# Performance work log

Hardware: AMD Instinct MI355X
Metric: run time of the kernel (lower is better)

The kernel has to match this reference:

```python
import jax, jax.numpy as jnp
import numpy as np

N, K, D, DOUT = 100000, 16, 128, 128

def setup_inputs() -> dict:
    key = jax.random.key(0)
    k1, k2, k3 = jax.random.split(key, 3)
    self_vecs = jax.random.normal(k1, (N, D), dtype=jnp.float32)
    neigh_vecs = jax.random.normal(k2, (N, K, D), dtype=jnp.float32)
    # glorot([input_dim, output_dim])
    limit = np.sqrt(6.0 / (D + DOUT)).astype(np.float32)
    weights = jax.random.uniform(k3, (D, DOUT), dtype=jnp.float32, minval=-limit, maxval=limit)
    return {"self_vecs": self_vecs, "neigh_vecs": neigh_vecs, "weights": weights}

def reference(self_vecs, neigh_vecs, weights):
    # concat self node as an extra "neighbor": [N, K+1, D]
    neigh_self = jnp.concatenate([neigh_vecs, self_vecs[:, None, :]], axis=1)
    # attention scores: query is the self vector, keys are neighbors+self -> [N, K+1]
    score = jnp.einsum('nd,nkd->nk', self_vecs, neigh_self)
    attn = jax.nn.softmax(score, axis=-1)
    # weighted sum of values -> [N, D]
    context = jnp.einsum('nk,nkd->nd', attn, neigh_self)
    out = context @ weights  # [N, DOUT]
    return jax.nn.relu(out)
```

## Files before the change

### kernel.cpp

```cpp
#include <hip/hip_runtime.h>


constexpr int K    = 16;
constexpr int D    = 128;
constexpr int DOUT = 128;
constexpr int CT_PITCH = 136;

typedef short bfrag  __attribute__((ext_vector_type(8)));
typedef float afrag  __attribute__((ext_vector_type(4)));
typedef float f32x4  __attribute__((ext_vector_type(4)));

__device__ __forceinline__ unsigned short f2bf(float f) {
    union { float f; unsigned u; } v; v.f = f;
    const unsigned r = v.u + 0x7FFF + ((v.u >> 16) & 1);
    return (unsigned short)(r >> 16);
}
__device__ __forceinline__ float bf2f(unsigned short b) {
    union { unsigned u; float f; } v; v.u = ((unsigned)b) << 16;
    return v.f;
}

__device__ __forceinline__ f32x4 nt_load4(const float* p) {
    return __builtin_nontemporal_load((const f32x4*)p);
}

__device__ __forceinline__ float half_allsum(float x) {
    #pragma unroll
    for (int off = 1; off <= 16; off <<= 1)
        x += __shfl_xor(x, off);
    return x;
}

__launch_bounds__(512, 2)
__global__ void gat_fused(const float* __restrict__ self_vecs,
                          const float* __restrict__ neigh_vecs,
                          const float* __restrict__ W,
                          float* __restrict__ out,
                          int n_stiles) {
    __shared__ __align__(16) unsigned short Chl[2][2][2][16][CT_PITCH];

    const int tid  = threadIdx.x;
    const int lane = tid & 63;
    const int wid  = tid >> 6;
    const int half = lane >> 5;
    const int q    = lane & 31;
    const int nl   = lane & 15;
    const int kb   = lane >> 4;
    const int r0   = wid * 2;

    bfrag a[4];
    #pragma unroll
    for (int kc = 0; kc < 4; ++kc)
        #pragma unroll
        for (int i = 0; i < 8; ++i) {
            const int k = kc * 32 + kb * 8 + i;
            a[kc][i] = (short)f2bf(W[k * DOUT + wid * 16 + nl]);
        }

    f32x4 v[K], sv;

    int buf = 0;
    int st = blockIdx.x;

    if (st < n_stiles) {
        const int n0 = st * 32 + r0 + half;
        const float* nb = neigh_vecs + (size_t)n0 * (K * D) + 4 * q;
        #pragma unroll
        for (int k = 0; k < K; ++k) v[k] = nt_load4(nb + k * D);
        sv = nt_load4(self_vecs + (size_t)n0 * D + 4 * q);
    }

    for (; st < n_stiles; st += gridDim.x, buf ^= 1) {
        #pragma unroll
        for (int tt = 0; tt < 2; ++tt) {
            int rs, rt;
            if (tt == 0) { rs = st; rt = 1; }
            else {
                const int sn = st + gridDim.x;
                rs = (sn < n_stiles) ? sn : st;
                rt = 0;
            }
            const int rn = (rs * 2 + rt) * 16 + r0 + half;
            const float* nbN = neigh_vecs + (size_t)rn * (K * D) + 4 * q;

            float ss = half_allsum(sv.x * sv.x + sv.y * sv.y + sv.z * sv.z + sv.w * sv.w);
            float sum = 1.f;
            f32x4 cx = sv;
            #pragma unroll
            for (int k = 0; k < K; ++k) {
                float p = sv.x * v[k].x + sv.y * v[k].y + sv.z * v[k].z + sv.w * v[k].w;
                p = half_allsum(p);
                const float e = __expf(p - ss);
                sum += e;
                cx.x += e * v[k].x; cx.y += e * v[k].y;
                cx.z += e * v[k].z; cx.w += e * v[k].w;
                v[k] = nt_load4(nbN + k * D);
            }
            sv = nt_load4(self_vecs + (size_t)rn * D + 4 * q);

            const float inv = 1.f / sum;
            const float cf[4] = {cx.x * inv, cx.y * inv, cx.z * inv, cx.w * inv};
            unsigned short hi4[4], lo4[4];
            #pragma unroll
            for (int i = 0; i < 4; ++i) {
                hi4[i] = f2bf(cf[i]);
                lo4[i] = f2bf(cf[i] - bf2f(hi4[i]));
            }
            *(uint2*)&Chl[buf][tt][0][r0 + half][4 * q] = *(const uint2*)hi4;
            *(uint2*)&Chl[buf][tt][1][r0 + half][4 * q] = *(const uint2*)lo4;
        }

        __syncthreads();

        #pragma unroll
        for (int tt = 0; tt < 2; ++tt) {
            afrag acc;
            #pragma unroll
            for (int r4 = 0; r4 < 4; ++r4) acc[r4] = 0.f;
            #pragma unroll
            for (int kc = 0; kc < 4; ++kc) {
                const bfrag ch = *(const bfrag*)&Chl[buf][tt][0][nl][kc * 32 + kb * 8];
                const bfrag cl = *(const bfrag*)&Chl[buf][tt][1][nl][kc * 32 + kb * 8];
                acc = __builtin_amdgcn_mfma_f32_16x16x32_bf16(a[kc], ch, acc, 0, 0, 0);
                acc = __builtin_amdgcn_mfma_f32_16x16x32_bf16(a[kc], cl, acc, 0, 0, 0);
            }
            const int node0t = (st * 2 + tt) * 16;
            float* orow = out + (size_t)(node0t + nl) * DOUT + kb * 4;
            f32x4 res;
            res.x = fmaxf(acc[0], 0.f); res.y = fmaxf(acc[1], 0.f);
            res.z = fmaxf(acc[2], 0.f); res.w = fmaxf(acc[3], 0.f);
            __builtin_nontemporal_store(res, (f32x4*)(orow + wid * 16));
        }
    }
}

extern "C" void kernel_launch(void* const* d_in, const int* in_sizes, int n_in,
                              void* d_out, int out_size, void* d_ws, size_t ws_size,
                              hipStream_t stream) {
    const float* self_vecs = (const float*)d_in[0];
    const float* neigh     = (const float*)d_in[1];
    const float* W         = (const float*)d_in[2];
    float* out = (float*)d_out;

    const int n_nodes  = in_sizes[0] / D;
    const int n_stiles = n_nodes / 32;

    const int tpb = 512;
    const int blocks = 512;
    gat_fused<<<dim3(blocks), dim3(tpb), 0, stream>>>(
        self_vecs, neigh, W, out, n_stiles);
}
```

Baseline: 172.5 us.

## Replace static grid-stride tile assignment with atomic work-queue dynamic scheduling

Blocks now take supertiles from a global atomic counter, kept in a workspace word and reset with a memset before each launch, instead of stepping by gridDim. The next tile is fetched one iteration ahead so the software prefetch of neighbor data still knows its target. This aims to balance load across blocks and cut tail imbalance, at the cost of an extra memset launch and an atomic per tile.

Result: slower. 180.0 us (+4.4%).

```diff
diff --git a/kernel.cpp b/kernel.cpp
--- a/kernel.cpp
+++ b/kernel.cpp
@@ -36,8 +36,9 @@
                           const float* __restrict__ neigh_vecs,
                           const float* __restrict__ W,
                           float* __restrict__ out,
-                          int n_stiles) {
+                          int n_stiles, int* __restrict__ qcnt) {
     __shared__ __align__(16) unsigned short Chl[2][2][2][16][CT_PITCH];
+    __shared__ int sQ[2];
 
     const int tid  = threadIdx.x;
     const int lane = tid & 63;
@@ -57,27 +58,32 @@
             a[kc][i] = (short)f2bf(W[k * DOUT + wid * 16 + nl]);
         }
 
+    if (tid == 0) {
+        sQ[0] = atomicAdd(qcnt, 1);
+        sQ[1] = atomicAdd(qcnt, 1);
+    }
+    __syncthreads();
+    int s_cur = sQ[0];
+    int s_nxt = sQ[1];
+
     f32x4 v[K], sv;
 
-    int buf = 0;
-    int st = blockIdx.x;
-
-    if (st < n_stiles) {
-        const int n0 = st * 32 + r0 + half;
+    if (s_cur < n_stiles) {
+        const int n0 = s_cur * 32 + r0 + half;
         const float* nb = neigh_vecs + (size_t)n0 * (K * D) + 4 * q;
         #pragma unroll
         for (int k = 0; k < K; ++k) v[k] = nt_load4(nb + k * D);
         sv = nt_load4(self_vecs + (size_t)n0 * D + 4 * q);
     }
 
-    for (; st < n_stiles; st += gridDim.x, buf ^= 1) {
+    int buf = 0, r = 0;
+    while (s_cur < n_stiles) {
         #pragma unroll
         for (int tt = 0; tt < 2; ++tt) {
             int rs, rt;
-            if (tt == 0) { rs = st; rt = 1; }
+            if (tt == 0) { rs = s_cur; rt = 1; }
             else {
-                const int sn = st + gridDim.x;
-                rs = (sn < n_stiles) ? sn : st;
+                rs = (s_nxt < n_stiles) ? s_nxt : s_cur;
                 rt = 0;
             }
             const int rn = (rs * 2 + rt) * 16 + r0 + half;
@@ -110,6 +116,8 @@
             *(uint2*)&Chl[buf][tt][1][r0 + half][4 * q] = *(const uint2*)lo4;
         }
 
+        if (tid == 0) sQ[r & 1] = atomicAdd(qcnt, 1);
+
         __syncthreads();
 
         #pragma unroll
@@ -124,13 +132,17 @@
                 acc = __builtin_amdgcn_mfma_f32_16x16x32_bf16(a[kc], ch, acc, 0, 0, 0);
                 acc = __builtin_amdgcn_mfma_f32_16x16x32_bf16(a[kc], cl, acc, 0, 0, 0);
             }
-            const int node0t = (st * 2 + tt) * 16;
+            const int node0t = (s_cur * 2 + tt) * 16;
             float* orow = out + (size_t)(node0t + nl) * DOUT + kb * 4;
             f32x4 res;
             res.x = fmaxf(acc[0], 0.f); res.y = fmaxf(acc[1], 0.f);
             res.z = fmaxf(acc[2], 0.f); res.w = fmaxf(acc[3], 0.f);
             __builtin_nontemporal_store(res, (f32x4*)(orow + wid * 16));
         }
+
+        s_cur = s_nxt;
+        s_nxt = sQ[r & 1];
+        buf ^= 1; ++r;
     }
 }
 
@@ -141,12 +153,15 @@
     const float* neigh     = (const float*)d_in[1];
     const float* W         = (const float*)d_in[2];
     float* out = (float*)d_out;
+    int* qcnt  = (int*)d_ws;
 
     const int n_nodes  = in_sizes[0] / D;
     const int n_stiles = n_nodes / 32;
 
+    hipMemsetAsync(qcnt, 0, sizeof(int), stream);
+
     const int tpb = 512;
     const int blocks = 512;
     gat_fused<<<dim3(blocks), dim3(tpb), 0, stream>>>(
-        self_vecs, neigh, W, out, n_stiles);
+        self_vecs, neigh, W, out, n_stiles, qcnt);
 }
```
